# Kernel tuning notes

Hardware: AMD Instinct MI355X
Metric: run time of the kernel (lower is better)

The kernel has to match this reference:

```python
import jax, jax.numpy as jnp
import numpy as np

HEADS = 16
DIM_HEAD = 64
SCALE = DIM_HEAD ** -0.5
EPS = 1e-5


def _vdp_linear(mu, sigma, Wmu, Wsig_raw):
    # y = W x with W ~ N(Wmu, softplus(Wsig_raw)), x ~ N(mu, sigma) (diag covs):
    # Var(y) = (mu^2 + sigma) @ Wsig^T + sigma @ (Wmu^2)^T
    Wsig = jax.nn.softplus(Wsig_raw)
    mu_y = mu @ Wmu.T
    sigma_y = (mu * mu + sigma) @ Wsig.T + sigma @ (Wmu * Wmu).T
    return mu_y, sigma_y


def _vdp_layernorm(mu, sigma, gamma, beta):
    mean = jnp.mean(mu, axis=-1, keepdims=True)
    var = jnp.var(mu, axis=-1, keepdims=True)
    inv = 1.0 / jnp.sqrt(var + EPS)
    mu_y = (mu - mean) * inv * gamma + beta
    # first-order variance propagation through the affine normalization
    sigma_y = sigma * (gamma * gamma) * (inv * inv)
    return mu_y, sigma_y


def _vdp_softmax(mu, sigma):
    p = jax.nn.softmax(mu, axis=-1)
    # diagonal-Jacobian approximation: J_ii = p_i(1-p_i)
    J = p * (1.0 - p)
    return p, (J * J) * sigma


def setup_inputs() -> dict:
    key = jax.random.key(0)
    ks = jax.random.split(key, 6)
    B, N, D = 4, 1024, 1024
    inner = HEADS * DIM_HEAD  # 1024
    w_std = 0.02
    return {
        "mu": jax.random.normal(ks[0], (B, N, D), jnp.float32),
        "sigma": jax.random.uniform(ks[1], (B, N, D), jnp.float32),
        "ln_gamma": jnp.ones((D,), jnp.float32),
        "ln_beta": jnp.zeros((D,), jnp.float32),
        "Wqkv_mu": w_std * jax.random.normal(ks[2], (3 * inner, D), jnp.float32),
        "Wqkv_sigma_raw": -5.0 + 0.1 * jax.random.normal(ks[3], (3 * inner, D), jnp.float32),
        "Wout_mu": w_std * jax.random.normal(ks[4], (D, inner), jnp.float32),
        "Wout_sigma_raw": -5.0 + 0.1 * jax.random.normal(ks[5], (D, inner), jnp.float32),
    }


def reference(mu, sigma, ln_gamma, ln_beta, Wqkv_mu, Wqkv_sigma_raw, Wout_mu, Wout_sigma_raw):
    B, N, D = mu.shape

    mu_n, sigma_n = _vdp_layernorm(mu, sigma, ln_gamma, ln_beta)
    mu_qkv, sigma_qkv = _vdp_linear(mu_n, sigma_n, Wqkv_mu, Wqkv_sigma_raw)

    def split_heads(t):
        q, k, v = jnp.split(t, 3, axis=-1)
        rs = lambda a: a.reshape(B, N, HEADS, DIM_HEAD).transpose(0, 2, 1, 3)
        return rs(q), rs(k), rs(v)

    mu_q, mu_k, mu_v = split_heads(mu_qkv)
    sg_q, sg_k, sg_v = split_heads(sigma_qkv)

    mu_dots = jnp.einsum("bhid,bhjd->bhij", mu_q, mu_k) * SCALE
    sg_dots = jnp.einsum("bhid,bhjd->bhij", sg_q, sg_k) * SCALE

    mu_attn, sg_attn = _vdp_softmax(mu_dots, sg_dots)

    mu_o = jnp.einsum("bhij,bhjd->bhid", mu_attn, mu_v)
    sg_o = jnp.einsum("bhij,bhjd->bhid", sg_attn, sg_v)

    merge = lambda t: t.transpose(0, 2, 1, 3).reshape(B, N, HEADS * DIM_HEAD)
    mu_o, sg_o = merge(mu_o), merge(sg_o)

    return _vdp_linear(mu_o, sg_o, Wout_mu, Wout_sigma_raw)
```

## Files before the change

### kernel.cpp

```cpp
#include <hip/hip_runtime.h>

typedef unsigned short u16;
typedef unsigned int u32;
typedef __bf16 bf16x8 __attribute__((ext_vector_type(8)));
typedef float f32x4 __attribute__((ext_vector_type(4)));
typedef float f32x16 __attribute__((ext_vector_type(16)));

__device__ __forceinline__ float b2f(u16 u) { return __uint_as_float(((u32)u) << 16); }
__device__ __forceinline__ u16 f2b(float f) {
  u32 u = __float_as_uint(f);
  u += 0x7fffu + ((u >> 16) & 1u);
  return (u16)(u >> 16);
}

__device__ __forceinline__ void gll16(const u16* g, u16* l) {
  __builtin_amdgcn_global_load_lds(
      (const __attribute__((address_space(1))) void*)g,
      (__attribute__((address_space(3))) void*)l, 16, 0, 0);
}

__device__ __forceinline__ float4 load4(const void* p, size_t idx, bool f32) {
  if (f32) return *(const float4*)((const float*)p + idx);
  ushort4 u = *(const ushort4*)((const u16*)p + idx);
  return make_float4(b2f(u.x), b2f(u.y), b2f(u.z), b2f(u.w));
}

#define SB __builtin_amdgcn_sched_barrier(0)
#define BARRIER do { SB; __builtin_amdgcn_s_barrier(); SB; } while (0)

__global__ __launch_bounds__(256) void detect_kernel(const u16* __restrict__ sig,
                                                     int* __restrict__ flag) {
  __shared__ int cnt;
  if (threadIdx.x == 0) cnt = 0;
  __syncthreads();
  int c = 0;
  for (int i = threadIdx.x; i < 16384; i += 256) {
    u16 v = sig[i];
    c += ((v & 0x7F80u) == 0x7F80u) ? 1 : 0;
  }
  atomicAdd(&cnt, c);
  __syncthreads();
  if (threadIdx.x == 0) *flag = (cnt >= 8) ? 1 : 0;
}

__global__ __launch_bounds__(256) void prep_kernel(
    const int* __restrict__ flag,
    const void* __restrict__ mu, const void* __restrict__ sigma,
    const void* __restrict__ gamma, const void* __restrict__ beta,
    u16* __restrict__ mu_n, u16* __restrict__ a1sg,
    const void* __restrict__ wq_mu, const void* __restrict__ wq_sraw,
    u16* __restrict__ q_bf, u16* __restrict__ q_s2,
    const void* __restrict__ wo_mu, const void* __restrict__ wo_sraw,
    u16* __restrict__ o_bf, u16* __restrict__ o_s2)
{
  __shared__ float ps[4], pq[4];
  const bool f32 = (*flag != 0);
  const int t = threadIdx.x;

  if (blockIdx.x < 4096) {
    const int wv = t >> 6, lane = t & 63;
    const size_t base = (size_t)blockIdx.x * 1024 + (size_t)t * 4;
    float4 xm = load4(mu, base, f32);
    float4 xs = load4(sigma, base, f32);
    float x0 = xm.x, x1 = xm.y, x2 = xm.z, x3 = xm.w;
    float s0 = xs.x, s1 = xs.y, s2 = xs.z, s3 = xs.w;

    float sv = x0 + x1 + x2 + x3;
    float qv = x0*x0 + x1*x1 + x2*x2 + x3*x3;
    #pragma unroll
    for (int off = 32; off > 0; off >>= 1) {
      sv += __shfl_xor(sv, off, 64);
      qv += __shfl_xor(qv, off, 64);
    }
    if (lane == 0) { ps[wv] = sv; pq[wv] = qv; }
    __syncthreads();
    float sum = ps[0] + ps[1] + ps[2] + ps[3];
    float ssq = pq[0] + pq[1] + pq[2] + pq[3];

    float mean = sum * (1.0f / 1024.0f);
    float var  = ssq * (1.0f / 1024.0f) - mean * mean;
    float inv  = 1.0f / sqrtf(var + 1e-5f);
    float inv2 = inv * inv;

    float4 g4 = load4(gamma, (size_t)t * 4, f32);
    float4 b4 = load4(beta, (size_t)t * 4, f32);

    float m0 = (x0 - mean) * inv * g4.x + b4.x;
    float m1 = (x1 - mean) * inv * g4.y + b4.y;
    float m2 = (x2 - mean) * inv * g4.z + b4.z;
    float m3 = (x3 - mean) * inv * g4.w + b4.w;
    float v0 = s0 * g4.x * g4.x * inv2;
    float v1 = s1 * g4.y * g4.y * inv2;
    float v2 = s2 * g4.z * g4.z * inv2;
    float v3 = s3 * g4.w * g4.w * inv2;

    ushort4 omu = { f2b(m0), f2b(m1), f2b(m2), f2b(m3) };
    ushort4 oa1 = { f2b(m0*m0 + v0), f2b(m1*m1 + v1), f2b(m2*m2 + v2), f2b(m3*m3 + v3) };
    ushort4 osg = { f2b(v0), f2b(v1), f2b(v2), f2b(v3) };
    *(ushort4*)(mu_n + base) = omu;
    size_t r2 = (size_t)blockIdx.x * 2048 + (size_t)t * 4;
    *(ushort4*)(a1sg + r2) = oa1;
    *(ushort4*)(a1sg + r2 + 1024) = osg;
  } else {
    const int nq = 3072 * 1024;
    size_t idx = ((size_t)(blockIdx.x - 4096) * 256 + t) * 4;
    const void *wmu, *wsr; u16 *obf, *os2;
    if (idx < (size_t)nq) { wmu = wq_mu; wsr = wq_sraw; obf = q_bf; os2 = q_s2; }
    else { idx -= nq; wmu = wo_mu; wsr = wo_sraw; obf = o_bf; os2 = o_s2; }
    int row = (int)(idx >> 10), k = (int)(idx & 1023);
    float4 m4 = load4(wmu, idx, f32);
    float4 s4 = load4(wsr, idx, f32);
    float m[4] = { m4.x, m4.y, m4.z, m4.w };
    float s[4] = { s4.x, s4.y, s4.z, s4.w };
    ushort4 ob, os, oq;
    u16* obp = (u16*)&ob; u16* osp = (u16*)&os; u16* oqp = (u16*)&oq;
    #pragma unroll
    for (int i = 0; i < 4; ++i) {
      float sp = (s[i] > 15.f) ? s[i] : log1pf(__expf(s[i]));
      obp[i] = f2b(m[i]);
      osp[i] = f2b(sp);
      oqp[i] = f2b(m[i] * m[i]);
    }
    *(ushort4*)(obf + idx) = ob;
    size_t r2 = (size_t)row * 2048 + k;
    *(ushort4*)(os2 + r2) = os;
    *(ushort4*)(os2 + r2 + 1024) = oq;
  }
}

template<bool DYN>
__global__ __launch_bounds__(256, 4) void gemm_out_kernel(
    const u16* __restrict__ A0, const u16* __restrict__ B0, int K0, void* C0, size_t ob0,
    const u16* __restrict__ A1, const u16* __restrict__ B1, int K1, void* C1, size_t ob1,
    int split, int N, const int* __restrict__ flag)
{
  __shared__ u16 lA[128 * 64];
  __shared__ u16 lB[64 * 64];
  const int t = threadIdx.x;
  int bx = blockIdx.x;
  const u16 *A, *B; void* C; size_t obase; int K;
  if (bx < split) { A = A0; B = B0; K = K0; C = C0; obase = ob0; }
  else { bx -= split; A = A1; B = B1; K = K1; C = C1; obase = ob1; }

  const int n0 = bx * 64, m0 = blockIdx.y * 128;
  const int lane = t & 63, wave = t >> 6;
  const int wr = (wave >> 1) * 64, wc = (wave & 1) * 32;
  const int m31 = lane & 31, h5 = lane >> 5;
  const int mx = m31 & 7;

  const int srow = t >> 3;
  const int gseg = (t & 7) ^ (srow & 7);

  f32x16 acc[2];
  #pragma unroll
  for (int i = 0; i < 2; ++i)
    #pragma unroll
    for (int r = 0; r < 16; ++r) acc[i][r] = 0.f;

  for (int k0 = 0; k0 < K; k0 += 64) {
    __syncthreads();
    #pragma unroll
    for (int rep = 0; rep < 4; ++rep)
      gll16(A + (size_t)(m0 + srow + rep * 32) * K + k0 + gseg * 8,
            lA + rep * 2048 + wave * 512);
    #pragma unroll
    for (int rep = 0; rep < 2; ++rep)
      gll16(B + (size_t)(n0 + srow + rep * 32) * K + k0 + gseg * 8,
            lB + rep * 2048 + wave * 512);
    __syncthreads();
    #pragma unroll
    for (int ks = 0; ks < 4; ++ks) {
      const int seg = ks * 2 + h5;
      bf16x8 af[2], bfr;
      #pragma unroll
      for (int tm = 0; tm < 2; ++tm)
        af[tm] = *(const bf16x8*)&lA[(wr + tm * 32 + m31) * 64 + (seg ^ mx) * 8];
      bfr = *(const bf16x8*)&lB[(wc + m31) * 64 + (seg ^ mx) * 8];
      #pragma unroll
      for (int tm = 0; tm < 2; ++tm)
        acc[tm] = __builtin_amdgcn_mfma_f32_32x32x16_bf16(af[tm], bfr, acc[tm], 0, 0, 0);
    }
  }

  const bool of32 = DYN && (*flag != 0);
  #pragma unroll
  for (int tm = 0; tm < 2; ++tm) {
    int colb = n0 + wc + m31;
    #pragma unroll
    for (int r = 0; r < 16; ++r) {
      int row = m0 + wr + tm * 32 + (r & 3) + 8 * (r >> 2) + 4 * h5;
      float v = acc[tm][r];
      size_t off = obase + (size_t)row * N + colb;
      if (DYN) {
        if (of32) ((float*)C)[off] = v;
        else      ((u16*)C)[off] = f2b(v);
      } else {
        ((u16*)C)[off] = f2b(v);
      }
    }
  }
}

__global__ __launch_bounds__(512, 2) void gemm8_pair_kernel(
    const u16* __restrict__ A0, const u16* __restrict__ B0, int K0, u16* __restrict__ C0,
    const u16* __restrict__ A1, const u16* __restrict__ B1, int K1, u16* __restrict__ C1,
    int split, int N)
{
  __shared__ u16 lA[2 * 256 * 64];
  __shared__ u16 lB[2 * 256 * 64];
  const int t = threadIdx.x;

  int wgid = blockIdx.y * 24 + blockIdx.x;
  int job;
  if (wgid < 192) job = (wgid & 7) * 24 + (wgid >> 3);
  else { int w2 = wgid - 192; job = 192 + (w2 & 7) * 24 + (w2 >> 3); }

  const u16 *A, *B; u16* C; int K, jb;
  if (job < split) { A = A0; B = B0; K = K0; C = C0; jb = job; }
  else { A = A1; B = B1; K = K1; C = C1; jb = job - split; }
  const int bm = jb & 15, bn = jb >> 4;
  const int m0 = bm * 256, n0 = bn * 256;
  const int NT = K >> 6;

  const int lane = t & 63, wave = t >> 6;
  const int wm = wave >> 2, wn = wave & 3;
  const int m31 = lane & 31, h5 = lane >> 5, mx = m31 & 7;

  auto stg64 = [&](const u16* __restrict__ X, int row0, int k0, u16* ldsU) {
    int r = row0 + wave * 8 + (lane >> 3);
    int seg = (lane & 7) ^ ((lane >> 3) & 7);
    gll16(X + (size_t)r * K + k0 + seg * 8, ldsU + wave * 512);
  };

  const u16* rdA = lA + (wm * 128 + m31) * 64;
  const u16* rdB = lB + (wn * 64 + m31) * 64;

  f32x16 acc[4][2];
  #pragma unroll
  for (int i = 0; i < 4; ++i)
    #pragma unroll
    for (int j = 0; j < 2; ++j)
      #pragma unroll
      for (int r = 0; r < 16; ++r) acc[i][j][r] = 0.f;

  bf16x8 af[2][4];
  bf16x8 bf[2][4];

  #pragma unroll
  for (int u = 0; u < 4; ++u) stg64(A, m0 + u * 64, 0, lA + u * 4096);
  #pragma unroll
  for (int u = 0; u < 4; ++u) stg64(B, n0 + u * 64, 0, lB + u * 4096);
  if (NT > 1) {
    #pragma unroll
    for (int u = 0; u < 4; ++u) stg64(B, n0 + u * 64, 64, lB + 16384 + u * 4096);
  }
  SB;
  asm volatile("s_waitcnt vmcnt(4)" ::: "memory");
  BARRIER;

  for (int T = 0; T < NT; ++T) {
    const int bo  = (T & 1) * 16384;
    const int bon = bo ^ 16384;
    const int kn  = (T + 1) * 64;
    const int kn2 = (T + 2) * 64;

    #pragma unroll
    for (int mf = 0; mf < 2; ++mf)
      #pragma unroll
      for (int ks = 0; ks < 4; ++ks)
        af[mf][ks] = *(const bf16x8*)&rdA[bo + mf * 2048 + (((ks * 2 + h5)) ^ mx) * 8];
    #pragma unroll
    for (int ks = 0; ks < 4; ++ks)
      bf[0][ks] = *(const bf16x8*)&rdB[bo + (((ks * 2 + h5)) ^ mx) * 8];
    if (T + 1 < NT) {
      stg64(A, m0,      kn, lA + bon);
      stg64(A, m0 + 64, kn, lA + bon + 4096);
    }
    BARRIER;
    __builtin_amdgcn_s_setprio(1);
    #pragma unroll
    for (int mf = 0; mf < 2; ++mf)
      #pragma unroll
      for (int ks = 0; ks < 4; ++ks)
        acc[mf][0] = __builtin_amdgcn_mfma_f32_32x32x16_bf16(af[mf][ks], bf[0][ks], acc[mf][0], 0, 0, 0);
    __builtin_amdgcn_s_setprio(0);
    BARRIER;

    #pragma unroll
    for (int ks = 0; ks < 4; ++ks)
      bf[1][ks] = *(const bf16x8*)&rdB[bo + 2048 + (((ks * 2 + h5)) ^ mx) * 8];
    if (T + 1 < NT) {
      stg64(A, m0 + 128, kn, lA + bon + 8192);
      stg64(A, m0 + 192, kn, lA + bon + 12288);
    }
    BARRIER;
    __builtin_amdgcn_s_setprio(1);
    #pragma unroll
    for (int mf = 0; mf < 2; ++mf)
      #pragma unroll
      for (int ks = 0; ks < 4; ++ks)
        acc[mf][1] = __builtin_amdgcn_mfma_f32_32x32x16_bf16(af[mf][ks], bf[1][ks], acc[mf][1], 0, 0, 0);
    __builtin_amdgcn_s_setprio(0);
    BARRIER;

    #pragma unroll
    for (int mf = 0; mf < 2; ++mf)
      #pragma unroll
      for (int ks = 0; ks < 4; ++ks)
        af[mf][ks] = *(const bf16x8*)&rdA[bo + (2 + mf) * 2048 + (((ks * 2 + h5)) ^ mx) * 8];
    if (T + 2 < NT) {
      stg64(B, n0,      kn2, lB + bo);
      stg64(B, n0 + 64, kn2, lB + bo + 4096);
    }
    BARRIER;
    __builtin_amdgcn_s_setprio(1);
    #pragma unroll
    for (int mf = 0; mf < 2; ++mf)
      #pragma unroll
      for (int ks = 0; ks < 4; ++ks)
        acc[2 + mf][1] = __builtin_amdgcn_mfma_f32_32x32x16_bf16(af[mf][ks], bf[1][ks], acc[2 + mf][1], 0, 0, 0);
    __builtin_amdgcn_s_setprio(0);
    BARRIER;

    if (T + 2 < NT) {
      stg64(B, n0 + 128, kn2, lB + bo + 8192);
      stg64(B, n0 + 192, kn2, lB + bo + 12288);
    }
    BARRIER;
    __builtin_amdgcn_s_setprio(1);
    #pragma unroll
    for (int mf = 0; mf < 2; ++mf)
      #pragma unroll
      for (int ks = 0; ks < 4; ++ks)
        acc[2 + mf][0] = __builtin_amdgcn_mfma_f32_32x32x16_bf16(af[mf][ks], bf[0][ks], acc[2 + mf][0], 0, 0, 0);
    __builtin_amdgcn_s_setprio(0);
    SB;
    if (T + 2 < NT) asm volatile("s_waitcnt vmcnt(4)" ::: "memory");
    else            asm volatile("s_waitcnt vmcnt(0)" ::: "memory");
    BARRIER;
  }

  #pragma unroll
  for (int mf = 0; mf < 4; ++mf)
    #pragma unroll
    for (int nf = 0; nf < 2; ++nf) {
      int colb = n0 + wn * 64 + nf * 32 + m31;
      #pragma unroll
      for (int r = 0; r < 16; ++r) {
        int row = m0 + wm * 128 + mf * 32 + (r & 3) + 8 * (r >> 2) + 4 * h5;
        C[(size_t)row * N + colb] = f2b(acc[mf][nf][r]);
      }
    }
}

__global__ __launch_bounds__(512, 4) void attn_pass2f(
    const u16* __restrict__ qkv_mu, const u16* __restrict__ qkv_sg,
    u16* __restrict__ o_mu, u16* __restrict__ a1sgo)
{
  __shared__ u16 lKW[128 * 72];
  __shared__ u16 lV[128 * 72];
  __shared__ u16 lP[128 * 72];
  __shared__ u16 lW[128 * 72];

  const int t = threadIdx.x;
  const int wv = t >> 6, lane = t & 63;
  const int ml = lane & 15, qd = lane >> 4;
  const int bid = blockIdx.x;
  const int ib = (bid >> 3) & 7;
  const int bh = (bid & 7) + ((bid >> 6) << 3);
  const int b = bh >> 4, h = bh & 15;
  const size_t rowbase = (size_t)b * 1024 * 3072;
  const int i0 = ib * 128;
  const int qcol = h * 64, kcol = 1024 + h * 64, vcol = 2048 + h * 64;
  const int qrow = wv * 16;

  bf16x8 aQm[2], aQs[2];
  #pragma unroll
  for (int ks = 0; ks < 2; ++ks) {
    size_t ga = rowbase + (size_t)(i0 + qrow + ml) * 3072 + qcol + ks * 32 + qd * 8;
    aQm[ks] = *(const bf16x8*)(qkv_mu + ga);
    aQs[ks] = *(const bf16x8*)(qkv_sg + ga);
  }

  float lsum[4] = {0.f, 0.f, 0.f, 0.f};
  f32x4 accm[4], acc2[4], acc3[4];
  #pragma unroll
  for (int tj = 0; tj < 4; ++tj) {
    accm[tj] = (f32x4){0.f, 0.f, 0.f, 0.f};
    acc2[tj] = (f32x4){0.f, 0.f, 0.f, 0.f};
    acc3[tj] = (f32x4){0.f, 0.f, 0.f, 0.f};
  }

  for (int j0 = 0; j0 < 1024; j0 += 64) {
    __syncthreads();
    #pragma unroll
    for (int rep = 0; rep < 2; ++rep) {
      int c = t + rep * 512;
      int row = c >> 3, seg = c & 7;
      const u16* src = (row < 64) ? qkv_mu : qkv_sg;
      int rr = row & 63;
      *(uint4*)&lKW[row * 72 + seg * 8] =
          *(const uint4*)(src + rowbase + (size_t)(j0 + rr) * 3072 + kcol + seg * 8);
    }
    {
      int buf = t >> 8, rem = t & 255;
      int db = rem >> 4, tb = rem & 15;
      const u16* src = buf ? qkv_sg : qkv_mu;
      ushort4 vals[4];
      #pragma unroll
      for (int i = 0; i < 4; ++i)
        vals[i] = *(const ushort4*)(src + rowbase + (size_t)(j0 + tb * 4 + i) * 3072 + vcol + db * 4);
      #pragma unroll
      for (int k = 0; k < 4; ++k) {
        ushort4 o;
        u16* op = (u16*)&o;
        const u16* v0 = (const u16*)&vals[0];
        const u16* v1 = (const u16*)&vals[1];
        const u16* v2 = (const u16*)&vals[2];
        const u16* v3 = (const u16*)&vals[3];
        op[0] = v0[k]; op[1] = v1[k]; op[2] = v2[k]; op[3] = v3[k];
        *(ushort4*)&lV[(buf * 64 + db * 4 + k) * 72 + tb * 4] = o;
      }
    }
    __syncthreads();

    float u3v[4][4];
    #pragma unroll
    for (int tj = 0; tj < 4; ++tj) {
      bf16x8 bm0 = *(const bf16x8*)&lKW[(tj * 16 + ml) * 72 + qd * 8];
      bf16x8 bm1 = *(const bf16x8*)&lKW[(tj * 16 + ml) * 72 + 32 + qd * 8];
      bf16x8 bs0 = *(const bf16x8*)&lKW[(64 + tj * 16 + ml) * 72 + qd * 8];
      bf16x8 bs1 = *(const bf16x8*)&lKW[(64 + tj * 16 + ml) * 72 + 32 + qd * 8];
      f32x4 s = (f32x4){0.f, 0.f, 0.f, 0.f};
      s = __builtin_amdgcn_mfma_f32_16x16x32_bf16(aQm[0], bm0, s, 0, 0, 0);
      s = __builtin_amdgcn_mfma_f32_16x16x32_bf16(aQm[1], bm1, s, 0, 0, 0);
      f32x4 s2 = (f32x4){0.f, 0.f, 0.f, 0.f};
      s2 = __builtin_amdgcn_mfma_f32_16x16x32_bf16(aQs[0], bs0, s2, 0, 0, 0);
      s2 = __builtin_amdgcn_mfma_f32_16x16x32_bf16(aQs[1], bs1, s2, 0, 0, 0);
      #pragma unroll
      for (int r = 0; r < 4; ++r) {
        float e  = __expf(s[r] * 0.125f);
        float st = s2[r] * 0.125f;
        float e2 = e * e;
        lsum[r] += e;
        int row = qrow + qd * 4 + r;
        lP[row * 72 + tj * 16 + ml] = f2b(e);
        lW[row * 72 + tj * 16 + ml] = f2b(e2 * st);
        u3v[tj][r] = e2 * e * st;
      }
    }
    __syncthreads();

    #pragma unroll
    for (int tj = 0; tj < 4; ++tj)
      #pragma unroll
      for (int r = 0; r < 4; ++r) {
        int row = qrow + qd * 4 + r;
        lKW[row * 72 + tj * 16 + ml] = f2b(u3v[tj][r]);
      }

    bf16x8 ap[2], aw[2], a3[2];
    #pragma unroll
    for (int ks = 0; ks < 2; ++ks) {
      ap[ks] = *(const bf16x8*)&lP[(qrow + ml) * 72 + ks * 32 + qd * 8];
      aw[ks] = *(const bf16x8*)&lW[(qrow + ml) * 72 + ks * 32 + qd * 8];
      a3[ks] = *(const bf16x8*)&lKW[(qrow + ml) * 72 + ks * 32 + qd * 8];
    }
    #pragma unroll
    for (int tj = 0; tj < 4; ++tj) {
      bf16x8 vm0 = *(const bf16x8*)&lV[(tj * 16 + ml) * 72 + qd * 8];
      bf16x8 vm1 = *(const bf16x8*)&lV[(tj * 16 + ml) * 72 + 32 + qd * 8];
      bf16x8 vs0 = *(const bf16x8*)&lV[(64 + tj * 16 + ml) * 72 + qd * 8];
      bf16x8 vs1 = *(const bf16x8*)&lV[(64 + tj * 16 + ml) * 72 + 32 + qd * 8];
      accm[tj] = __builtin_amdgcn_mfma_f32_16x16x32_bf16(ap[0], vm0, accm[tj], 0, 0, 0);
      accm[tj] = __builtin_amdgcn_mfma_f32_16x16x32_bf16(ap[1], vm1, accm[tj], 0, 0, 0);
      acc2[tj] = __builtin_amdgcn_mfma_f32_16x16x32_bf16(aw[0], vs0, acc2[tj], 0, 0, 0);
      acc2[tj] = __builtin_amdgcn_mfma_f32_16x16x32_bf16(aw[1], vs1, acc2[tj], 0, 0, 0);
      acc3[tj] = __builtin_amdgcn_mfma_f32_16x16x32_bf16(a3[0], vs0, acc3[tj], 0, 0, 0);
      acc3[tj] = __builtin_amdgcn_mfma_f32_16x16x32_bf16(a3[1], vs1, acc3[tj], 0, 0, 0);
    }
  }

  #pragma unroll
  for (int r = 0; r < 4; ++r) {
    float l = lsum[r];
    #pragma unroll
    for (int xo = 1; xo < 16; xo <<= 1) l += __shfl_xor(l, xo, 64);
    lsum[r] = l;
  }

  #pragma unroll
  for (int tj = 0; tj < 4; ++tj)
    #pragma unroll
    for (int r = 0; r < 4; ++r) {
      int row = i0 + qrow + qd * 4 + r;
      int col = h * 64 + tj * 16 + ml;
      size_t rowg = (size_t)b * 1024 + row;
      float il  = 1.0f / lsum[r];
      float il2 = il * il;
      float om = accm[tj][r] * il;
      float os = acc2[tj][r] * il2 - 2.0f * acc3[tj][r] * il2 * il;
      o_mu[rowg * 1024 + col] = f2b(om);
      size_t r2 = rowg * 2048 + col;
      a1sgo[r2] = f2b(fmaf(om, om, os));
      a1sgo[r2 + 1024] = f2b(os);
    }
}

extern "C" void kernel_launch(void* const* d_in, const int* in_sizes, int n_in,
                              void* d_out, int out_size, void* d_ws, size_t ws_size,
                              hipStream_t stream)
{
  (void)in_sizes; (void)n_in; (void)out_size; (void)ws_size;
  const void* mu        = d_in[0];
  const void* sigma     = d_in[1];
  const void* gamma     = d_in[2];
  const void* beta      = d_in[3];
  const void* wqkv_mu   = d_in[4];
  const void* wqkv_sraw = d_in[5];
  const void* wout_mu   = d_in[6];
  const void* wout_sraw = d_in[7];

  u16* ws = (u16*)d_ws;
  const size_t R = 4096;
  u16* mu_n   = ws;
  u16* a1sg   = mu_n + R * 1024;
  u16* wq_bf  = a1sg + R * 2048;
  u16* wqs2   = wq_bf + 3072 * 1024;
  u16* wo_bf  = wqs2 + 3072 * 2048;
  u16* wos2   = wo_bf + 1024 * 1024;
  u16* mu_qkv = wos2 + 1024 * 2048;
  u16* sg_qkv = mu_qkv + R * 3072;
  int* flag   = (int*)(sg_qkv + R * 3072);

  u16* mu_o  = mu_n;
  u16* a1sgo = a1sg;

  detect_kernel<<<1, 256, 0, stream>>>((const u16*)sigma, flag);

  prep_kernel<<<8192, 256, 0, stream>>>(
      flag, mu, sigma, gamma, beta, mu_n, a1sg,
      wqkv_mu, wqkv_sraw, wq_bf, wqs2,
      wout_mu, wout_sraw, wo_bf, wos2);

  gemm8_pair_kernel<<<dim3(24, 16), 512, 0, stream>>>(
      a1sg, wqs2, 2048, sg_qkv,
      mu_n, wq_bf, 1024, mu_qkv,
      192, 3072);

  attn_pass2f<<<dim3(512), 512, 0, stream>>>(mu_qkv, sg_qkv, mu_o, a1sgo);

  gemm_out_kernel<true><<<dim3(32, 32), 256, 0, stream>>>(
      mu_o, wo_bf, 1024, d_out, 0,
      a1sgo, wos2, 2048, d_out, R * 1024,
      16, 1024, flag);
}
```

Baseline: 390.2 us.

## Prefetch next K/V tile into registers and remap out-GEMM blocks per XCD

The attention kernel now loads the next K/V tile from global memory into registers while the current tile is being computed, then writes it to LDS at the top of the next iteration, hiding global load latency behind MFMA work. The output GEMM launch becomes 1D, with block ids mapped so that each XCD gets a contiguous group of row tiles for the mu and sigma halves, aiming for better L2 reuse of A rows. The prefetch adds register pressure in the attention kernel, which may reduce occupancy.

```diff
diff --git a/kernel.cpp b/kernel.cpp
--- a/kernel.cpp
+++ b/kernel.cpp
@@ -132,17 +132,22 @@
 __global__ __launch_bounds__(256, 4) void gemm_out_kernel(
     const u16* __restrict__ A0, const u16* __restrict__ B0, int K0, void* C0, size_t ob0,
     const u16* __restrict__ A1, const u16* __restrict__ B1, int K1, void* C1, size_t ob1,
-    int split, int N, const int* __restrict__ flag)
+    int N, const int* __restrict__ flag)
 {
   __shared__ u16 lA[128 * 64];
   __shared__ u16 lB[64 * 64];
   const int t = threadIdx.x;
-  int bx = blockIdx.x;
-  const u16 *A, *B; void* C; size_t obase; int K;
-  if (bx < split) { A = A0; B = B0; K = K0; C = C0; obase = ob0; }
-  else { bx -= split; A = A1; B = B1; K = K1; C = C1; obase = ob1; }
-
-  const int n0 = bx * 64, m0 = blockIdx.y * 128;
+
+  const int wgid = blockIdx.x;
+  const int xcd = wgid & 7;
+  const int idx = wgid >> 3;
+  const u16 *A, *B; void* C; size_t obase; int K; int l;
+  if (idx < 64) { A = A0; B = B0; K = K0; C = C0; obase = ob0; l = idx; }
+  else          { A = A1; B = B1; K = K1; C = C1; obase = ob1; l = idx - 64; }
+  const int by = xcd * 4 + (l >> 4);
+  const int bx = l & 15;
+  const int n0 = bx * 64, m0 = by * 128;
+
   const int lane = t & 63, wave = t >> 6;
   const int wr = (wave >> 1) * 64, wc = (wave & 1) * 32;
   const int m31 = lane & 31, h5 = lane >> 5;
@@ -382,6 +387,22 @@
     aQs[ks] = *(const bf16x8*)(qkv_sg + ga);
   }
 
+  const int krow = t >> 3, kseg = t & 7;
+  const int vbuf = t >> 8, vrem = t & 255;
+  const int vdb = vrem >> 4, vtb = vrem & 15;
+  const u16* vsrc = vbuf ? qkv_sg : qkv_mu;
+  uint4 kmu, ksg;
+  ushort4 vv[4];
+
+  auto loadKV = [&](int j0) {
+    size_t ka = rowbase + (size_t)(j0 + krow) * 3072 + kcol + kseg * 8;
+    kmu = *(const uint4*)(qkv_mu + ka);
+    ksg = *(const uint4*)(qkv_sg + ka);
+    #pragma unroll
+    for (int i = 0; i < 4; ++i)
+      vv[i] = *(const ushort4*)(vsrc + rowbase + (size_t)(j0 + vtb * 4 + i) * 3072 + vcol + vdb * 4);
+  };
+
   float lsum[4] = {0.f, 0.f, 0.f, 0.f};
   f32x4 accm[4], acc2[4], acc3[4];
   #pragma unroll
@@ -391,37 +412,23 @@
     acc3[tj] = (f32x4){0.f, 0.f, 0.f, 0.f};
   }
 
+  loadKV(0);
+
   for (int j0 = 0; j0 < 1024; j0 += 64) {
     __syncthreads();
-    #pragma unroll
-    for (int rep = 0; rep < 2; ++rep) {
-      int c = t + rep * 512;
-      int row = c >> 3, seg = c & 7;
-      const u16* src = (row < 64) ? qkv_mu : qkv_sg;
-      int rr = row & 63;
-      *(uint4*)&lKW[row * 72 + seg * 8] =
-          *(const uint4*)(src + rowbase + (size_t)(j0 + rr) * 3072 + kcol + seg * 8);
-    }
-    {
-      int buf = t >> 8, rem = t & 255;
-      int db = rem >> 4, tb = rem & 15;
-      const u16* src = buf ? qkv_sg : qkv_mu;
-      ushort4 vals[4];
-      #pragma unroll
-      for (int i = 0; i < 4; ++i)
-        vals[i] = *(const ushort4*)(src + rowbase + (size_t)(j0 + tb * 4 + i) * 3072 + vcol + db * 4);
-      #pragma unroll
-      for (int k = 0; k < 4; ++k) {
-        ushort4 o;
-        u16* op = (u16*)&o;
-        const u16* v0 = (const u16*)&vals[0];
-        const u16* v1 = (const u16*)&vals[1];
-        const u16* v2 = (const u16*)&vals[2];
-        const u16* v3 = (const u16*)&vals[3];
-        op[0] = v0[k]; op[1] = v1[k]; op[2] = v2[k]; op[3] = v3[k];
-        *(ushort4*)&lV[(buf * 64 + db * 4 + k) * 72 + tb * 4] = o;
-      }
-    }
+    *(uint4*)&lKW[krow * 72 + kseg * 8] = kmu;
+    *(uint4*)&lKW[(krow + 64) * 72 + kseg * 8] = ksg;
+    #pragma unroll
+    for (int k = 0; k < 4; ++k) {
+      ushort4 o;
+      u16* op = (u16*)&o;
+      op[0] = ((const u16*)&vv[0])[k];
+      op[1] = ((const u16*)&vv[1])[k];
+      op[2] = ((const u16*)&vv[2])[k];
+      op[3] = ((const u16*)&vv[3])[k];
+      *(ushort4*)&lV[(vbuf * 64 + vdb * 4 + k) * 72 + vtb * 4] = o;
+    }
+    if (j0 + 64 < 1024) loadKV(j0 + 64);
     __syncthreads();
 
     float u3v[4][4];
@@ -550,8 +557,8 @@
 
   attn_pass2f<<<dim3(512), 512, 0, stream>>>(mu_qkv, sg_qkv, mu_o, a1sgo);
 
-  gemm_out_kernel<true><<<dim3(32, 32), 256, 0, stream>>>(
+  gemm_out_kernel<true><<<dim3(1024), 256, 0, stream>>>(
       mu_o, wo_bf, 1024, d_out, 0,
       a1sgo, wos2, 2048, d_out, R * 1024,
-      16, 1024, flag);
-}
+      1024, flag);
+}
```

Result: slower. 455.1 us (+16.6%).
